# Kernel tuning notes

Measured on AMD Instinct MI355X. Metric: run time of the kernel, lower is better.

Reference implementation:

```python
import jax, jax.numpy as jnp
import numpy as np

N_NODES = 100000
HIDDEN = 128
N_EDGES = 1000000


def setup_inputs() -> dict:
    key = jax.random.key(0)
    k1, k2, k3, k4 = jax.random.split(key, 4)
    z = jax.random.normal(k1, (N_NODES, HIDDEN), dtype=jnp.float32)
    edge_label_index = jax.random.randint(k2, (2, N_EDGES), 0, N_NODES, dtype=jnp.int64)
    # Kaiming-ish scaled init for the two Linear layers (lin1: 2H->H, lin2: H->1)
    W1 = jax.random.normal(k3, (2 * HIDDEN, HIDDEN), dtype=jnp.float32) / np.sqrt(2 * HIDDEN)
    b1 = jnp.zeros((HIDDEN,), dtype=jnp.float32)
    W2 = jax.random.normal(k4, (HIDDEN, 1), dtype=jnp.float32) / np.sqrt(HIDDEN)
    b2 = jnp.zeros((1,), dtype=jnp.float32)
    return {"z": z, "edge_label_index": edge_label_index, "W1": W1, "b1": b1, "W2": W2, "b2": b2}


def reference(z, edge_label_index, W1, b1, W2, b2):
    row, col = edge_label_index[0], edge_label_index[1]
    # gather endpoint embeddings and concat: [E, 2H]
    h = jnp.concatenate([z[row], z[col]], axis=-1)
    h = jax.nn.relu(h @ W1 + b1)          # [E, H]
    out = h @ W2 + b2                     # [E, 1]
    return out.reshape(-1)
```

## Files before the change

### kernel.cpp

```cpp
#include <hip/hip_runtime.h>
#include <hip/hip_bf16.h>
#include <stdint.h>

#define HIDDEN 128
#define LDS_STRIDE 136

typedef __attribute__((ext_vector_type(8))) short short8;
typedef __attribute__((ext_vector_type(4))) unsigned uint4v;
typedef __attribute__((ext_vector_type(4))) float float4v;
typedef __attribute__((ext_vector_type(2))) float float2v;
typedef __attribute__((ext_vector_type(2))) unsigned uint2v;

static __device__ __forceinline__ unsigned short f2bf(float f) {
    union { float f; unsigned u; } v; v.f = f;
    unsigned r = (v.u + 0x7FFFu + ((v.u >> 16) & 1u)) >> 16;
    return (unsigned short)r;
}

static __device__ __forceinline__ unsigned pack2bf(float f0, float f1) {
    unsigned u0 = __float_as_uint(f0) + 0x8000u;
    unsigned u1 = __float_as_uint(f1) + 0x8000u;
    return __builtin_amdgcn_perm(u1, u0, 0x07060302u);
}

static __device__ __forceinline__ short8 pack8(float4v lo, float4v hi) {
    uint4v u;
    u[0] = pack2bf(lo[0], lo[1]);
    u[1] = pack2bf(lo[2], lo[3]);
    u[2] = pack2bf(hi[0], hi[1]);
    u[3] = pack2bf(hi[2], hi[3]);
    return *(short8*)&u;
}

__global__ void prep_wt(const float* __restrict__ W1, const float* __restrict__ b1,
                        const float* __restrict__ W2,
                        unsigned short* __restrict__ Wt,
                        float* __restrict__ b1p, float* __restrict__ W2p) {
    int idx = blockIdx.x * blockDim.x + threadIdx.x;
    if (idx < 256 * 128) {
        int j = idx >> 7, k = idx & 127;
        float v = (j < 128) ? W1[k * 128 + j] : W1[(128 + k) * 128 + (j - 128)];
        Wt[idx] = f2bf(v);
    }
    if (idx < 128) {
        int m = idx >> 3, tt = idx & 7;
        int jj = tt * 16 + m;
        b1p[idx] = b1[jj];
        W2p[idx] = W2[jj];
    }
}

__global__ __launch_bounds__(512) void node_gemm(
        const float* __restrict__ z, const unsigned short* __restrict__ Wt,
        const float* __restrict__ b1p,
        unsigned char* __restrict__ Qi, float* __restrict__ sA, float* __restrict__ sB,
        int n_nodes) {
    __shared__ unsigned short Wl[128 * LDS_STRIDE];

    int tid  = threadIdx.x;
    int h    = blockIdx.x & 1;
    int lane = tid & 63;
    int wave = tid >> 6;
    int m    = lane & 15;
    int quad = lane >> 4;

    int nTiles   = (n_nodes + 15) >> 4;
    int tile     = (blockIdx.x >> 1) * 8 + wave;
    bool active  = tile < nTiles;
    int nodebase = tile * 16;
    int row      = nodebase + m;

    float4v zr[8];
    {
        bool ok = active && (row < n_nodes);
        const float* zp = z + (size_t)row * HIDDEN + quad * 8;
        #pragma unroll
        for (int s = 0; s < 4; ++s) {
            zr[2 * s]     = ok ? *(const float4v*)(zp + s * 32)     : (float4v)(0.0f);
            zr[2 * s + 1] = ok ? *(const float4v*)(zp + s * 32 + 4) : (float4v)(0.0f);
        }
    }

    #pragma unroll
    for (int i = 0; i < 4; ++i) {
        int chunk = tid + i * 512;
        int c  = chunk >> 4;
        int k0 = (chunk & 15) * 8;
        short8 v = *(const short8*)(Wt + h * 16384 + chunk * 8);
        *(short8*)(Wl + c * LDS_STRIDE + k0) = v;
    }
    __syncthreads();
    if (!active) return;

    float4v b1a = (float4v)(0.0f), b1b = (float4v)(0.0f);
    if (h == 0) {
        b1a = *(const float4v*)(b1p + m * 8);
        b1b = *(const float4v*)(b1p + m * 8 + 4);
    }
    float* sArr = (h == 0) ? sA : sB;

    short8 a[4];
    #pragma unroll
    for (int s = 0; s < 4; ++s) a[s] = pack8(zr[2 * s], zr[2 * s + 1]);

    float4v acc[8];
    #pragma unroll
    for (int t = 0; t < 8; ++t) acc[t] = (float4v)(0.0f);

    #pragma unroll
    for (int t = 0; t < 8; ++t) {
        const unsigned short* wp = Wl + (t * 16 + m) * LDS_STRIDE + quad * 8;
        #pragma unroll
        for (int s = 0; s < 4; ++s) {
            short8 b = *(const short8*)(wp + s * 32);
            acc[t] = __builtin_amdgcn_mfma_f32_16x16x32_bf16(a[s], b, acc[t], 0, 0, 0);
        }
    }

    #pragma unroll
    for (int r = 0; r < 4; ++r) {
        int node = nodebase + quad * 4 + r;
        float v[8];
        v[0] = acc[0][r] + b1a[0]; v[1] = acc[1][r] + b1a[1];
        v[2] = acc[2][r] + b1a[2]; v[3] = acc[3][r] + b1a[3];
        v[4] = acc[4][r] + b1b[0]; v[5] = acc[5][r] + b1b[1];
        v[6] = acc[6][r] + b1b[2]; v[7] = acc[7][r] + b1b[3];

        float amax = fabsf(v[0]);
        #pragma unroll
        for (int t = 1; t < 8; ++t) amax = fmaxf(amax, fabsf(v[t]));
        amax = fmaxf(amax, __shfl_xor(amax, 1));
        amax = fmaxf(amax, __shfl_xor(amax, 2));
        amax = fmaxf(amax, __shfl_xor(amax, 4));
        amax = fmaxf(amax, __shfl_xor(amax, 8));
        amax = fmaxf(amax, 1e-30f);

        float inv = 126.5f * __builtin_amdgcn_rcpf(amax);
        float s   = amax * (1.0f / 126.5f);

        unsigned d0 = 0, d1 = 0;
        #pragma unroll
        for (int t = 0; t < 4; ++t) {
            int q = (int)rintf(fmaf(v[t], inv, 128.0f));
            d0 |= ((unsigned)q & 255u) << (8 * t);
        }
        #pragma unroll
        for (int t = 0; t < 4; ++t) {
            int q = (int)rintf(fmaf(v[4 + t], inv, 128.0f));
            d1 |= ((unsigned)q & 255u) << (8 * t);
        }

        if (node < n_nodes) {
            uint2v pk; pk[0] = d0; pk[1] = d1;
            *(uint2v*)(Qi + (size_t)node * 256 + h * 128 + m * 8) = pk;
            if (m == 0) sArr[node] = s;
        }
    }
}

static __device__ __forceinline__ float edge_dot8(uint2v u1, uint2v u2,
                                                  float a1, float a2,
                                                  const float2v* w2) {
    float offs = -128.0f * (a1 + a2);
    float2v off2; off2[0] = offs; off2[1] = offs;
    float2v a1v;  a1v[0] = a1;   a1v[1] = a1;
    float2v a2v;  a2v[0] = a2;   a2v[1] = a2;
    float2v acc2; acc2[0] = 0.0f; acc2[1] = 0.0f;
    #pragma unroll
    for (int d = 0; d < 2; ++d) {
        unsigned da = u1[d], db = u2[d];
        #pragma unroll
        for (int p = 0; p < 2; ++p) {
            float2v af, bf;
            af[0] = (float)((da >> (16 * p))     & 255u);
            af[1] = (float)((da >> (16 * p + 8)) & 255u);
            bf[0] = (float)((db >> (16 * p))     & 255u);
            bf[1] = (float)((db >> (16 * p + 8)) & 255u);
            float2v t = a2v * bf + off2;
            float2v s = a1v * af + t;
            s[0] = fmaxf(s[0], 0.0f);
            s[1] = fmaxf(s[1], 0.0f);
            acc2 = acc2 + s * w2[2 * d + p];
        }
    }
    return acc2[0] + acc2[1];
}

__global__ __launch_bounds__(256) void edge_kernel(
        const int* __restrict__ eli, const unsigned char* __restrict__ Qi,
        const float* __restrict__ sA, const float* __restrict__ sB,
        const float* __restrict__ W2p, const float* __restrict__ b2,
        float* __restrict__ out, int E) {
    int g      = threadIdx.x >> 4;
    int lane16 = threadIdx.x & 15;
    int j0 = lane16 * 8;

    float2v w2[4];
    #pragma unroll
    for (int k = 0; k < 4; ++k) w2[k] = ((const float2v*)(W2p + j0))[k];
    float bias2 = b2[0];

    int e0 = blockIdx.x * 64 + g;

    int idx_r[4], idx_c[4];
    #pragma unroll
    for (int i = 0; i < 4; ++i) {
        int e = e0 + i * 16;
        idx_r[i] = (e < E) ? eli[e]     : 0;
        idx_c[i] = (e < E) ? eli[E + e] : 0;
    }

    uint2v u1[4], u2[4];
    float s1[4], s2[4];
    #pragma unroll
    for (int i = 0; i < 4; ++i) {
        u1[i] = *(const uint2v*)(Qi + (size_t)idx_r[i] * 256 + j0);
        u2[i] = *(const uint2v*)(Qi + (size_t)idx_c[i] * 256 + 128 + j0);
        s1[i] = sA[idx_r[i]];
        s2[i] = sB[idx_c[i]];
    }

    #pragma unroll
    for (int i = 0; i < 4; ++i) {
        float acc = edge_dot8(u1[i], u2[i], s1[i], s2[i], w2);
        acc += __shfl_xor(acc, 1);
        acc += __shfl_xor(acc, 2);
        acc += __shfl_xor(acc, 4);
        acc += __shfl_xor(acc, 8);
        int e = e0 + i * 16;
        if (lane16 == 0 && e < E)
            __builtin_nontemporal_store(acc + bias2, &out[e]);
    }
}

extern "C" void kernel_launch(void* const* d_in, const int* in_sizes, int n_in,
                              void* d_out, int out_size, void* d_ws, size_t ws_size,
                              hipStream_t stream) {
    const float* z   = (const float*)d_in[0];
    const int*   eli = (const int*)d_in[1];
    const float* W1  = (const float*)d_in[2];
    const float* b1  = (const float*)d_in[3];
    const float* W2  = (const float*)d_in[4];
    const float* b2  = (const float*)d_in[5];
    int n_nodes = in_sizes[0] / HIDDEN;
    int E       = in_sizes[1] / 2;
    float* out  = (float*)d_out;

    size_t off = 0;
    unsigned char* Qi  = (unsigned char*)d_ws;                 off += (size_t)n_nodes * 256;
    unsigned short* Wt = (unsigned short*)((char*)d_ws + off); off += 256 * 128 * 2;
    float* b1p = (float*)((char*)d_ws + off);                  off += 128 * 4;
    float* W2p = (float*)((char*)d_ws + off);                  off += 128 * 4;
    float* sA  = (float*)((char*)d_ws + off);                  off += (size_t)n_nodes * 4;
    float* sB  = (float*)((char*)d_ws + off);                  off += (size_t)n_nodes * 4;

    prep_wt<<<128, 256, 0, stream>>>(W1, b1, W2, Wt, b1p, W2p);

    int nTiles = (n_nodes + 15) / 16;
    int blocksPerHalf = (nTiles + 7) / 8;
    node_gemm<<<2 * blocksPerHalf, 512, 0, stream>>>(z, Wt, b1p, Qi, sA, sB, n_nodes);

    edge_kernel<<<(E + 63) / 64, 256, 0, stream>>>(eli, Qi, sA, sB, W2p, b2, out, E);
}
```

Baseline: 160.7 us.

## Compute both weight halves per node block and batch eight edges per group

The node GEMM now loads the full 256x128 bf16 weight into LDS using an XOR swizzle instead of padding, and loops over both halves in one block. Each z tile is therefore read once rather than twice, at the cost of doubled LDS (64KB) and lower occupancy. The edge kernel processes 8 consecutive edges per 16-lane group, so all gathers are issued up front, and writes results with vectorized float4 stores instead of scalar nontemporal stores.

```diff
diff --git a/kernel.cpp b/kernel.cpp
--- a/kernel.cpp
+++ b/kernel.cpp
@@ -3,7 +3,6 @@
 #include <stdint.h>
 
 #define HIDDEN 128
-#define LDS_STRIDE 136
 
 typedef __attribute__((ext_vector_type(8))) short short8;
 typedef __attribute__((ext_vector_type(4))) unsigned uint4v;
@@ -55,17 +54,16 @@
         const float* __restrict__ b1p,
         unsigned char* __restrict__ Qi, float* __restrict__ sA, float* __restrict__ sB,
         int n_nodes) {
-    __shared__ unsigned short Wl[128 * LDS_STRIDE];
+    __shared__ unsigned short Wl[2 * 128 * 128];
 
     int tid  = threadIdx.x;
-    int h    = blockIdx.x & 1;
     int lane = tid & 63;
     int wave = tid >> 6;
     int m    = lane & 15;
     int quad = lane >> 4;
 
     int nTiles   = (n_nodes + 15) >> 4;
-    int tile     = (blockIdx.x >> 1) * 8 + wave;
+    int tile     = blockIdx.x * 8 + wave;
     bool active  = tile < nTiles;
     int nodebase = tile * 16;
     int row      = nodebase + m;
@@ -82,78 +80,83 @@
     }
 
     #pragma unroll
-    for (int i = 0; i < 4; ++i) {
+    for (int i = 0; i < 8; ++i) {
         int chunk = tid + i * 512;
         int c  = chunk >> 4;
         int k0 = (chunk & 15) * 8;
-        short8 v = *(const short8*)(Wt + h * 16384 + chunk * 8);
-        *(short8*)(Wl + c * LDS_STRIDE + k0) = v;
+        short8 v = *(const short8*)(Wt + chunk * 8);
+        int off = c * 128 + k0;
+        *(short8*)(Wl + (off ^ ((c & 7) << 3))) = v;
     }
     __syncthreads();
     if (!active) return;
 
-    float4v b1a = (float4v)(0.0f), b1b = (float4v)(0.0f);
-    if (h == 0) {
-        b1a = *(const float4v*)(b1p + m * 8);
-        b1b = *(const float4v*)(b1p + m * 8 + 4);
-    }
-    float* sArr = (h == 0) ? sA : sB;
+    float4v b1a = *(const float4v*)(b1p + m * 8);
+    float4v b1b = *(const float4v*)(b1p + m * 8 + 4);
 
     short8 a[4];
     #pragma unroll
     for (int s = 0; s < 4; ++s) a[s] = pack8(zr[2 * s], zr[2 * s + 1]);
 
-    float4v acc[8];
-    #pragma unroll
-    for (int t = 0; t < 8; ++t) acc[t] = (float4v)(0.0f);
-
-    #pragma unroll
-    for (int t = 0; t < 8; ++t) {
-        const unsigned short* wp = Wl + (t * 16 + m) * LDS_STRIDE + quad * 8;
-        #pragma unroll
-        for (int s = 0; s < 4; ++s) {
-            short8 b = *(const short8*)(wp + s * 32);
-            acc[t] = __builtin_amdgcn_mfma_f32_16x16x32_bf16(a[s], b, acc[t], 0, 0, 0);
-        }
-    }
-
-    #pragma unroll
-    for (int r = 0; r < 4; ++r) {
-        int node = nodebase + quad * 4 + r;
-        float v[8];
-        v[0] = acc[0][r] + b1a[0]; v[1] = acc[1][r] + b1a[1];
-        v[2] = acc[2][r] + b1a[2]; v[3] = acc[3][r] + b1a[3];
-        v[4] = acc[4][r] + b1b[0]; v[5] = acc[5][r] + b1b[1];
-        v[6] = acc[6][r] + b1b[2]; v[7] = acc[7][r] + b1b[3];
-
-        float amax = fabsf(v[0]);
-        #pragma unroll
-        for (int t = 1; t < 8; ++t) amax = fmaxf(amax, fabsf(v[t]));
-        amax = fmaxf(amax, __shfl_xor(amax, 1));
-        amax = fmaxf(amax, __shfl_xor(amax, 2));
-        amax = fmaxf(amax, __shfl_xor(amax, 4));
-        amax = fmaxf(amax, __shfl_xor(amax, 8));
-        amax = fmaxf(amax, 1e-30f);
-
-        float inv = 126.5f * __builtin_amdgcn_rcpf(amax);
-        float s   = amax * (1.0f / 126.5f);
-
-        unsigned d0 = 0, d1 = 0;
-        #pragma unroll
-        for (int t = 0; t < 4; ++t) {
-            int q = (int)rintf(fmaf(v[t], inv, 128.0f));
-            d0 |= ((unsigned)q & 255u) << (8 * t);
-        }
-        #pragma unroll
-        for (int t = 0; t < 4; ++t) {
-            int q = (int)rintf(fmaf(v[4 + t], inv, 128.0f));
-            d1 |= ((unsigned)q & 255u) << (8 * t);
-        }
-
-        if (node < n_nodes) {
-            uint2v pk; pk[0] = d0; pk[1] = d1;
-            *(uint2v*)(Qi + (size_t)node * 256 + h * 128 + m * 8) = pk;
-            if (m == 0) sArr[node] = s;
+    #pragma unroll
+    for (int h = 0; h < 2; ++h) {
+        float4v acc[8];
+        #pragma unroll
+        for (int t = 0; t < 8; ++t) acc[t] = (float4v)(0.0f);
+
+        int swz = (m & 7) << 3;
+        #pragma unroll
+        for (int t = 0; t < 8; ++t) {
+            int base = (h * 128 + t * 16 + m) * 128 + quad * 8;
+            #pragma unroll
+            for (int s = 0; s < 4; ++s) {
+                short8 b = *(const short8*)(Wl + ((base + s * 32) ^ swz));
+                acc[t] = __builtin_amdgcn_mfma_f32_16x16x32_bf16(a[s], b, acc[t], 0, 0, 0);
+            }
+        }
+
+        float4v ba = (h == 0) ? b1a : (float4v)(0.0f);
+        float4v bb = (h == 0) ? b1b : (float4v)(0.0f);
+        float* sArr = (h == 0) ? sA : sB;
+
+        #pragma unroll
+        for (int r = 0; r < 4; ++r) {
+            int node = nodebase + quad * 4 + r;
+            float v[8];
+            v[0] = acc[0][r] + ba[0]; v[1] = acc[1][r] + ba[1];
+            v[2] = acc[2][r] + ba[2]; v[3] = acc[3][r] + ba[3];
+            v[4] = acc[4][r] + bb[0]; v[5] = acc[5][r] + bb[1];
+            v[6] = acc[6][r] + bb[2]; v[7] = acc[7][r] + bb[3];
+
+            float amax = fabsf(v[0]);
+            #pragma unroll
+            for (int t = 1; t < 8; ++t) amax = fmaxf(amax, fabsf(v[t]));
+            amax = fmaxf(amax, __shfl_xor(amax, 1));
+            amax = fmaxf(amax, __shfl_xor(amax, 2));
+            amax = fmaxf(amax, __shfl_xor(amax, 4));
+            amax = fmaxf(amax, __shfl_xor(amax, 8));
+            amax = fmaxf(amax, 1e-30f);
+
+            float inv = 126.5f * __builtin_amdgcn_rcpf(amax);
+            float s   = amax * (1.0f / 126.5f);
+
+            unsigned d0 = 0, d1 = 0;
+            #pragma unroll
+            for (int t = 0; t < 4; ++t) {
+                int q = (int)rintf(fmaf(v[t], inv, 128.0f));
+                d0 |= ((unsigned)q & 255u) << (8 * t);
+            }
+            #pragma unroll
+            for (int t = 0; t < 4; ++t) {
+                int q = (int)rintf(fmaf(v[4 + t], inv, 128.0f));
+                d1 |= ((unsigned)q & 255u) << (8 * t);
+            }
+
+            if (node < n_nodes) {
+                uint2v pk; pk[0] = d0; pk[1] = d1;
+                *(uint2v*)(Qi + (size_t)node * 256 + h * 128 + m * 8) = pk;
+                if (m == 0) sArr[node] = s;
+            }
         }
     }
 }
@@ -193,43 +196,60 @@
         float* __restrict__ out, int E) {
     int g      = threadIdx.x >> 4;
     int lane16 = threadIdx.x & 15;
-    int j0 = lane16 * 8;
+    int j0     = lane16 * 8;
 
     float2v w2[4];
     #pragma unroll
     for (int k = 0; k < 4; ++k) w2[k] = ((const float2v*)(W2p + j0))[k];
     float bias2 = b2[0];
 
-    int e0 = blockIdx.x * 64 + g;
-
-    int idx_r[4], idx_c[4];
-    #pragma unroll
-    for (int i = 0; i < 4; ++i) {
-        int e = e0 + i * 16;
-        idx_r[i] = (e < E) ? eli[e]     : 0;
-        idx_c[i] = (e < E) ? eli[E + e] : 0;
-    }
-
-    uint2v u1[4], u2[4];
-    float s1[4], s2[4];
-    #pragma unroll
-    for (int i = 0; i < 4; ++i) {
+    int ebase = blockIdx.x * 128 + g * 8;
+
+    int idx_r[8], idx_c[8];
+    #pragma unroll
+    for (int i = 0; i < 8; ++i) {
+        int e = ebase + i;
+        bool ok = e < E;
+        idx_r[i] = ok ? eli[e]     : 0;
+        idx_c[i] = ok ? eli[E + e] : 0;
+    }
+
+    uint2v u1[8], u2[8];
+    #pragma unroll
+    for (int i = 0; i < 8; ++i) {
         u1[i] = *(const uint2v*)(Qi + (size_t)idx_r[i] * 256 + j0);
         u2[i] = *(const uint2v*)(Qi + (size_t)idx_c[i] * 256 + 128 + j0);
+    }
+    float s1[8], s2[8];
+    #pragma unroll
+    for (int i = 0; i < 8; ++i) {
         s1[i] = sA[idx_r[i]];
         s2[i] = sB[idx_c[i]];
     }
 
-    #pragma unroll
-    for (int i = 0; i < 4; ++i) {
+    float res[8];
+    #pragma unroll
+    for (int i = 0; i < 8; ++i) {
         float acc = edge_dot8(u1[i], u2[i], s1[i], s2[i], w2);
         acc += __shfl_xor(acc, 1);
         acc += __shfl_xor(acc, 2);
         acc += __shfl_xor(acc, 4);
         acc += __shfl_xor(acc, 8);
-        int e = e0 + i * 16;
-        if (lane16 == 0 && e < E)
-            __builtin_nontemporal_store(acc + bias2, &out[e]);
+        res[i] = acc + bias2;
+    }
+
+    if (lane16 == 0) {
+        if (ebase + 8 <= E) {
+            float4v r0, r1;
+            r0[0] = res[0]; r0[1] = res[1]; r0[2] = res[2]; r0[3] = res[3];
+            r1[0] = res[4]; r1[1] = res[5]; r1[2] = res[6]; r1[3] = res[7];
+            *(float4v*)(out + ebase)     = r0;
+            *(float4v*)(out + ebase + 4) = r1;
+        } else {
+            #pragma unroll
+            for (int i = 0; i < 8; ++i)
+                if (ebase + i < E) out[ebase + i] = res[i];
+        }
     }
 }
 
@@ -257,8 +277,7 @@
     prep_wt<<<128, 256, 0, stream>>>(W1, b1, W2, Wt, b1p, W2p);
 
     int nTiles = (n_nodes + 15) / 16;
-    int blocksPerHalf = (nTiles + 7) / 8;
-    node_gemm<<<2 * blocksPerHalf, 512, 0, stream>>>(z, Wt, b1p, Qi, sA, sB, n_nodes);
-
-    edge_kernel<<<(E + 63) / 64, 256, 0, stream>>>(eli, Qi, sA, sB, W2p, b2, out, E);
-}
+    node_gemm<<<(nTiles + 7) / 8, 512, 0, stream>>>(z, Wt, b1p, Qi, sA, sB, n_nodes);
+
+    edge_kernel<<<(E + 127) / 128, 256, 0, stream>>>(eli, Qi, sA, sB, W2p, b2, out, E);
+}
```

Result: no change. 158.6 us (-1.3%).
